# Performance work log

Hardware: AMD Instinct MI355X
Metric: run time of the kernel (lower is better)

The kernel has to match this reference:

```python
import jax
import jax.numpy as jnp
import numpy as np
from jax import lax


def setup_inputs() -> dict:
    key = jax.random.key(0)
    ks = jax.random.split(key, 8)
    B, T, D, H = 65536, 200, 6, 50
    scale1 = 1.0 / np.sqrt(D)
    scale2 = 1.0 / np.sqrt(H)
    return {
        "x0": jax.random.normal(ks[0], (B, T, D), dtype=jnp.float32),
        "t_span": jnp.linspace(0.0, 1.01, 102, dtype=jnp.float32),
        "W1": jax.random.normal(ks[1], (D, H), dtype=jnp.float32) * scale1,
        "b1": jax.random.normal(ks[2], (H,), dtype=jnp.float32) * scale1,
        "W2": jax.random.normal(ks[3], (H, H), dtype=jnp.float32) * scale2,
        "b2": jax.random.normal(ks[4], (H,), dtype=jnp.float32) * scale2,
        "W3": jax.random.normal(ks[5], (H, D), dtype=jnp.float32) * scale2,
        "b3": jax.random.normal(ks[6], (D,), dtype=jnp.float32) * scale2,
    }


def _mlp(y, W1, b1, W2, b2, W3, b3):
    # 3-layer MLP: 6 -> 50 -> 50 -> 6 with ReLU (the ODE dynamics f(t, y))
    h = jax.nn.relu(y @ W1 + b1)
    h = jax.nn.relu(h @ W2 + b2)
    return h @ W3 + b3


def reference(x0, t_span, W1, b1, W2, b2, W3, b3):
    # DimensionalityReduction: AdaptiveAvgPool1d(1) over the time axis == mean over T
    y0 = jnp.mean(x0, axis=1)  # [B, 6]

    def f(y):
        return _mlp(y, W1, b1, W2, b2, W3, b3)

    dts = t_span[1:] - t_span[:-1]  # [101]

    def rk4_step(y, dt):
        k1 = f(y)
        k2 = f(y + 0.5 * dt * k1)
        k3 = f(y + 0.5 * dt * k2)
        k4 = f(y + dt * k3)
        y_next = y + (dt / 6.0) * (k1 + 2.0 * k2 + 2.0 * k3 + k4)
        return y_next, None

    yT, _ = lax.scan(rk4_step, y0, dts)
    return yT  # y[-1], shape [B, 6]
```

## Files before the change

kernel.cpp:

```cpp
#include <hip/hip_runtime.h>
#include <cstdint>


#define D_IN   6
#define H_DIM  50
#define T_LEN  200

typedef const float __attribute__((address_space(4)))* cfp;

__device__ __forceinline__ void mlp_eval(
    cfp W1, cfp b1, cfp W2, cfp b2, cfp W3, cfp b3,
    const float y[D_IN], float k[D_IN])
{
    float h1[H_DIM];
#pragma unroll
    for (int j = 0; j < H_DIM; ++j) h1[j] = b1[j];
#pragma unroll
    for (int i = 0; i < D_IN; ++i) {
        float v = y[i];
#pragma unroll
        for (int j = 0; j < H_DIM; ++j) h1[j] = fmaf(v, W1[i * H_DIM + j], h1[j]);
    }
#pragma unroll
    for (int j = 0; j < H_DIM; ++j) h1[j] = fmaxf(h1[j], 0.0f);

    float h2[H_DIM];
#pragma unroll
    for (int j = 0; j < H_DIM; ++j) h2[j] = b2[j];
#pragma unroll
    for (int i = 0; i < H_DIM; ++i) {
        float v = h1[i];
#pragma unroll
        for (int j = 0; j < H_DIM; ++j) h2[j] = fmaf(v, W2[i * H_DIM + j], h2[j]);
    }

#pragma unroll
    for (int d = 0; d < D_IN; ++d) k[d] = b3[d];
#pragma unroll
    for (int i = 0; i < H_DIM; ++i) {
        float v = fmaxf(h2[i], 0.0f);
#pragma unroll
        for (int d = 0; d < D_IN; ++d) k[d] = fmaf(v, W3[i * D_IN + d], k[d]);
    }
}

extern "C" __global__ __launch_bounds__(256)
void ode_fused(const float* __restrict__ x0, const float* __restrict__ ts_g,
               const float* __restrict__ W1g, const float* __restrict__ b1g,
               const float* __restrict__ W2g, const float* __restrict__ b2g,
               const float* __restrict__ W3g, const float* __restrict__ b3g,
               float* __restrict__ out, int nt)
{
    int b = blockIdx.x * blockDim.x + threadIdx.x;

    cfp W1 = (cfp)(uintptr_t)W1g;
    cfp b1 = (cfp)(uintptr_t)b1g;
    cfp W2 = (cfp)(uintptr_t)W2g;
    cfp b2 = (cfp)(uintptr_t)b2g;
    cfp W3 = (cfp)(uintptr_t)W3g;
    cfp b3 = (cfp)(uintptr_t)b3g;
    cfp ts = (cfp)(uintptr_t)ts_g;

    const float4* xrow = (const float4*)(x0 + (size_t)b * (T_LEN * D_IN));
    float acc[D_IN];
#pragma unroll
    for (int d = 0; d < D_IN; ++d) acc[d] = 0.0f;

#pragma unroll 4
    for (int c = 0; c < (T_LEN * D_IN) / 12; ++c) {
        float4 v0 = xrow[c * 3 + 0];
        float4 v1 = xrow[c * 3 + 1];
        float4 v2 = xrow[c * 3 + 2];
        acc[0] += v0.x + v1.z;
        acc[1] += v0.y + v1.w;
        acc[2] += v0.z + v2.x;
        acc[3] += v0.w + v2.y;
        acc[4] += v1.x + v2.z;
        acc[5] += v1.y + v2.w;
    }

    float y[D_IN];
#pragma unroll
    for (int d = 0; d < D_IN; ++d) y[d] = acc[d] * (1.0f / (float)T_LEN);

#pragma unroll 1
    for (int s = 0; s < nt - 1; ++s) {
        float t0 = ts[s];
        float t1 = ts[s + 1];
        float dt = t1 - t0;

        float acck[D_IN];
        float yt[D_IN];
#pragma unroll
        for (int d = 0; d < D_IN; ++d) { acck[d] = 0.0f; yt[d] = y[d]; }

#pragma unroll 1
        for (int st = 0; st < 4; ++st) {
            float k[D_IN];
            mlp_eval(W1, b1, W2, b2, W3, b3, yt, k);
            float w = (st == 1 || st == 2) ? 2.0f : 1.0f;
            float a = (st == 2) ? 1.0f : 0.5f;
#pragma unroll
            for (int d = 0; d < D_IN; ++d) {
                acck[d] = fmaf(w, k[d], acck[d]);
                yt[d]   = fmaf(a * dt, k[d], y[d]);
            }
        }
#pragma unroll
        for (int d = 0; d < D_IN; ++d) y[d] = fmaf(dt * (1.0f / 6.0f), acck[d], y[d]);
    }

    float* o = out + (size_t)b * D_IN;
#pragma unroll
    for (int d = 0; d < D_IN; ++d) o[d] = y[d];
}

extern "C" void kernel_launch(void* const* d_in, const int* in_sizes, int n_in,
                              void* d_out, int out_size, void* d_ws, size_t ws_size,
                              hipStream_t stream) {
    const float* x0 = (const float*)d_in[0];
    const float* ts = (const float*)d_in[1];
    const float* W1 = (const float*)d_in[2];
    const float* b1 = (const float*)d_in[3];
    const float* W2 = (const float*)d_in[4];
    const float* b2 = (const float*)d_in[5];
    const float* W3 = (const float*)d_in[6];
    const float* b3 = (const float*)d_in[7];
    float* out = (float*)d_out;

    int B  = in_sizes[0] / (T_LEN * D_IN);
    int nt = in_sizes[1];

    dim3 block(256);
    dim3 grid(B / 256);
    hipLaunchKernelGGL(ode_fused, grid, block, 0, stream,
                       x0, ts, W1, b1, W2, b2, W3, b3, out, nt);
}
```

Measured before the change: 4.967 ms.

## Stage padded MLP weights in LDS and spill hidden layer to shared memory

Weights, biases and time points are copied once per block into padded LDS buffers, so the MLP reads weights as broadcast float4 LDS loads instead of scalar constant-memory loads. The first hidden activation is written to a per-thread strided LDS scratch and read back in a partially unrolled loop, which lowers register pressure in the 50x50 layer. The cost is extra LDS traffic per evaluation, about 54KB of LDS per block which limits occupancy, and a __launch_bounds__ hint of one block per CU.

```diff
diff --git a/kernel.cpp b/kernel.cpp
--- a/kernel.cpp
+++ b/kernel.cpp
@@ -3,69 +3,133 @@
 
 
 #define D_IN   6
-#define H_DIM  50
+#define H      50
+#define HP     52
+#define W3P    8
 #define T_LEN  200
-
-typedef const float __attribute__((address_space(4)))* cfp;
+#define NTHR   256
+
+#define OFF_W1 0
+#define OFF_B1 (OFF_W1 + D_IN*HP)
+#define OFF_W2 (OFF_B1 + HP)
+#define OFF_B2 (OFF_W2 + H*HP)
+#define OFF_W3 (OFF_B2 + HP)
+#define OFF_B3 (OFF_W3 + H*W3P)
+#define OFF_TS (OFF_B3 + W3P)
+#define OFF_H1 (OFF_TS + 104)
+#define SMEM_FLOATS (OFF_H1 + H*NTHR)
 
 __device__ __forceinline__ void mlp_eval(
-    cfp W1, cfp b1, cfp W2, cfp b2, cfp W3, cfp b3,
-    const float y[D_IN], float k[D_IN])
+    const float* __restrict__ sm, int tid, const float yt[D_IN], float k[D_IN])
 {
-    float h1[H_DIM];
-#pragma unroll
-    for (int j = 0; j < H_DIM; ++j) h1[j] = b1[j];
-#pragma unroll
-    for (int i = 0; i < D_IN; ++i) {
-        float v = y[i];
-#pragma unroll
-        for (int j = 0; j < H_DIM; ++j) h1[j] = fmaf(v, W1[i * H_DIM + j], h1[j]);
-    }
-#pragma unroll
-    for (int j = 0; j < H_DIM; ++j) h1[j] = fmaxf(h1[j], 0.0f);
-
-    float h2[H_DIM];
-#pragma unroll
-    for (int j = 0; j < H_DIM; ++j) h2[j] = b2[j];
-#pragma unroll
-    for (int i = 0; i < H_DIM; ++i) {
-        float v = h1[i];
-#pragma unroll
-        for (int j = 0; j < H_DIM; ++j) h2[j] = fmaf(v, W2[i * H_DIM + j], h2[j]);
-    }
-
-#pragma unroll
-    for (int d = 0; d < D_IN; ++d) k[d] = b3[d];
-#pragma unroll
-    for (int i = 0; i < H_DIM; ++i) {
+    float h1[HP];
+    {
+        const float4* B1 = (const float4*)(sm + OFF_B1);
+#pragma unroll
+        for (int q = 0; q < HP / 4; ++q) {
+            float4 v = B1[q];
+            h1[4 * q + 0] = v.x; h1[4 * q + 1] = v.y;
+            h1[4 * q + 2] = v.z; h1[4 * q + 3] = v.w;
+        }
+#pragma unroll
+        for (int i = 0; i < D_IN; ++i) {
+            float v = yt[i];
+            const float4* Wr = (const float4*)(sm + OFF_W1 + i * HP);
+#pragma unroll
+            for (int q = 0; q < HP / 4; ++q) {
+                float4 w = Wr[q];
+                h1[4 * q + 0] = fmaf(v, w.x, h1[4 * q + 0]);
+                h1[4 * q + 1] = fmaf(v, w.y, h1[4 * q + 1]);
+                h1[4 * q + 2] = fmaf(v, w.z, h1[4 * q + 2]);
+                h1[4 * q + 3] = fmaf(v, w.w, h1[4 * q + 3]);
+            }
+        }
+    }
+
+    float* e = (float*)(sm + OFF_H1) + tid;
+#pragma unroll
+    for (int j = 0; j < H; ++j) e[j * NTHR] = fmaxf(h1[j], 0.0f);
+
+    float h2[HP];
+    {
+        const float4* B2 = (const float4*)(sm + OFF_B2);
+#pragma unroll
+        for (int q = 0; q < HP / 4; ++q) {
+            float4 v = B2[q];
+            h2[4 * q + 0] = v.x; h2[4 * q + 1] = v.y;
+            h2[4 * q + 2] = v.z; h2[4 * q + 3] = v.w;
+        }
+    }
+#pragma unroll 2
+    for (int i = 0; i < H; ++i) {
+        float v = sm[OFF_H1 + i * NTHR + tid];
+        const float4* Wr = (const float4*)(sm + OFF_W2 + i * HP);
+#pragma unroll
+        for (int q = 0; q < HP / 4; ++q) {
+            float4 w = Wr[q];
+            h2[4 * q + 0] = fmaf(v, w.x, h2[4 * q + 0]);
+            h2[4 * q + 1] = fmaf(v, w.y, h2[4 * q + 1]);
+            h2[4 * q + 2] = fmaf(v, w.z, h2[4 * q + 2]);
+            h2[4 * q + 3] = fmaf(v, w.w, h2[4 * q + 3]);
+        }
+    }
+
+    {
+        const float4* B3 = (const float4*)(sm + OFF_B3);
+        float4 b30 = B3[0], b31 = B3[1];
+        k[0] = b30.x; k[1] = b30.y; k[2] = b30.z;
+        k[3] = b30.w; k[4] = b31.x; k[5] = b31.y;
+    }
+#pragma unroll
+    for (int i = 0; i < H; ++i) {
         float v = fmaxf(h2[i], 0.0f);
-#pragma unroll
-        for (int d = 0; d < D_IN; ++d) k[d] = fmaf(v, W3[i * D_IN + d], k[d]);
+        const float4* Wr = (const float4*)(sm + OFF_W3 + i * W3P);
+        float4 w0 = Wr[0], w1 = Wr[1];
+        k[0] = fmaf(v, w0.x, k[0]);
+        k[1] = fmaf(v, w0.y, k[1]);
+        k[2] = fmaf(v, w0.z, k[2]);
+        k[3] = fmaf(v, w0.w, k[3]);
+        k[4] = fmaf(v, w1.x, k[4]);
+        k[5] = fmaf(v, w1.y, k[5]);
     }
 }
 
-extern "C" __global__ __launch_bounds__(256)
+extern "C" __global__ __launch_bounds__(NTHR, 1)
 void ode_fused(const float* __restrict__ x0, const float* __restrict__ ts_g,
                const float* __restrict__ W1g, const float* __restrict__ b1g,
                const float* __restrict__ W2g, const float* __restrict__ b2g,
                const float* __restrict__ W3g, const float* __restrict__ b3g,
                float* __restrict__ out, int nt)
 {
-    int b = blockIdx.x * blockDim.x + threadIdx.x;
-
-    cfp W1 = (cfp)(uintptr_t)W1g;
-    cfp b1 = (cfp)(uintptr_t)b1g;
-    cfp W2 = (cfp)(uintptr_t)W2g;
-    cfp b2 = (cfp)(uintptr_t)b2g;
-    cfp W3 = (cfp)(uintptr_t)W3g;
-    cfp b3 = (cfp)(uintptr_t)b3g;
-    cfp ts = (cfp)(uintptr_t)ts_g;
+    __shared__ float sm[SMEM_FLOATS];
+    const int tid = threadIdx.x;
+    const int b   = blockIdx.x * NTHR + tid;
+
+    for (int idx = tid; idx < D_IN * HP; idx += NTHR) {
+        int r = idx / HP, c = idx - r * HP;
+        sm[OFF_W1 + idx] = (c < H) ? W1g[r * H + c] : 0.0f;
+    }
+    for (int idx = tid; idx < HP; idx += NTHR)
+        sm[OFF_B1 + idx] = (idx < H) ? b1g[idx] : 0.0f;
+    for (int idx = tid; idx < H * HP; idx += NTHR) {
+        int r = idx / HP, c = idx - r * HP;
+        sm[OFF_W2 + idx] = (c < H) ? W2g[r * H + c] : 0.0f;
+    }
+    for (int idx = tid; idx < HP; idx += NTHR)
+        sm[OFF_B2 + idx] = (idx < H) ? b2g[idx] : 0.0f;
+    for (int idx = tid; idx < H * W3P; idx += NTHR) {
+        int r = idx >> 3, c = idx & 7;
+        sm[OFF_W3 + idx] = (c < D_IN) ? W3g[r * D_IN + c] : 0.0f;
+    }
+    for (int idx = tid; idx < W3P; idx += NTHR)
+        sm[OFF_B3 + idx] = (idx < D_IN) ? b3g[idx] : 0.0f;
+    for (int idx = tid; idx < nt && idx < 104; idx += NTHR)
+        sm[OFF_TS + idx] = ts_g[idx];
 
     const float4* xrow = (const float4*)(x0 + (size_t)b * (T_LEN * D_IN));
     float acc[D_IN];
 #pragma unroll
     for (int d = 0; d < D_IN; ++d) acc[d] = 0.0f;
-
 #pragma unroll 4
     for (int c = 0; c < (T_LEN * D_IN) / 12; ++c) {
         float4 v0 = xrow[c * 3 + 0];
@@ -78,15 +142,16 @@
         acc[4] += v1.x + v2.z;
         acc[5] += v1.y + v2.w;
     }
-
     float y[D_IN];
 #pragma unroll
     for (int d = 0; d < D_IN; ++d) y[d] = acc[d] * (1.0f / (float)T_LEN);
+
+    __syncthreads();
 
 #pragma unroll 1
     for (int s = 0; s < nt - 1; ++s) {
-        float t0 = ts[s];
-        float t1 = ts[s + 1];
+        float t0 = sm[OFF_TS + s];
+        float t1 = sm[OFF_TS + s + 1];
         float dt = t1 - t0;
 
         float acck[D_IN];
@@ -97,7 +162,7 @@
 #pragma unroll 1
         for (int st = 0; st < 4; ++st) {
             float k[D_IN];
-            mlp_eval(W1, b1, W2, b2, W3, b3, yt, k);
+            mlp_eval(sm, tid, yt, k);
             float w = (st == 1 || st == 2) ? 2.0f : 1.0f;
             float a = (st == 2) ? 1.0f : 0.5f;
 #pragma unroll
@@ -131,8 +196,8 @@
     int B  = in_sizes[0] / (T_LEN * D_IN);
     int nt = in_sizes[1];
 
-    dim3 block(256);
-    dim3 grid(B / 256);
+    dim3 block(NTHR);
+    dim3 grid(B / NTHR);
     hipLaunchKernelGGL(ode_fused, grid, block, 0, stream,
                        x0, ts, W1, b1, W2, b2, W3, b3, out, nt);
 }
```

After: 8.404 ms. +69.2%, slower.

## Stage hidden activations in LDS and double-buffer vectorized W2 row-pair loads

Applied to the files above, without the earlier changes.

The MLP evaluation is restructured. Weights are now read as float4 vector loads through plain global pointers instead of scalar constant-address-space loads. The ReLU'd first hidden layer is spilled to a per-thread LDS column so the W2 product can stream two rows at a time through double-buffered register arrays. Launch bounds are raised to allow more registers per thread. The aim is to cut scalar-load instruction overhead and hide weight-load latency. The cost is 50 KB of LDS per block and lower occupancy, and weight loads move from the scalar path to per-lane vector loads.

```diff
diff --git a/kernel.cpp b/kernel.cpp
--- a/kernel.cpp
+++ b/kernel.cpp
@@ -3,69 +3,69 @@
 
 
 #define D_IN   6
-#define H_DIM  50
+#define H      50
 #define T_LEN  200
-
-typedef const float __attribute__((address_space(4)))* cfp;
-
-__device__ __forceinline__ void mlp_eval(
-    cfp W1, cfp b1, cfp W2, cfp b2, cfp W3, cfp b3,
-    const float y[D_IN], float k[D_IN])
+#define NTHR   256
+#define NPAIR  25
+
+__device__ __forceinline__ float f4c(float4 v, int c) {
+    return c == 0 ? v.x : c == 1 ? v.y : c == 2 ? v.z : v.w;
+}
+
+__device__ __forceinline__ void load_pair(float4 (&buf)[NPAIR], const float4* W2f4, int p,
+                                          float& v0, float& v1, const float* echoT)
 {
-    float h1[H_DIM];
-#pragma unroll
-    for (int j = 0; j < H_DIM; ++j) h1[j] = b1[j];
-#pragma unroll
-    for (int i = 0; i < D_IN; ++i) {
-        float v = y[i];
-#pragma unroll
-        for (int j = 0; j < H_DIM; ++j) h1[j] = fmaf(v, W1[i * H_DIM + j], h1[j]);
-    }
-#pragma unroll
-    for (int j = 0; j < H_DIM; ++j) h1[j] = fmaxf(h1[j], 0.0f);
-
-    float h2[H_DIM];
-#pragma unroll
-    for (int j = 0; j < H_DIM; ++j) h2[j] = b2[j];
-#pragma unroll
-    for (int i = 0; i < H_DIM; ++i) {
-        float v = h1[i];
-#pragma unroll
-        for (int j = 0; j < H_DIM; ++j) h2[j] = fmaf(v, W2[i * H_DIM + j], h2[j]);
-    }
-
-#pragma unroll
-    for (int d = 0; d < D_IN; ++d) k[d] = b3[d];
-#pragma unroll
-    for (int i = 0; i < H_DIM; ++i) {
-        float v = fmaxf(h2[i], 0.0f);
-#pragma unroll
-        for (int d = 0; d < D_IN; ++d) k[d] = fmaf(v, W3[i * D_IN + d], k[d]);
-    }
-}
-
-extern "C" __global__ __launch_bounds__(256)
+    const float4* w = W2f4 + p * NPAIR;
+#pragma unroll
+    for (int q = 0; q < NPAIR; ++q) buf[q] = w[q];
+    v0 = echoT[(2 * p) * NTHR];
+    v1 = echoT[(2 * p + 1) * NTHR];
+}
+
+__device__ __forceinline__ void fma_pair(const float4 (&buf)[NPAIR], float v0, float v1,
+                                         float (&h2)[H])
+{
+#pragma unroll
+    for (int q = 0; q < 12; ++q) {
+        h2[4 * q + 0] = fmaf(v0, buf[q].x, h2[4 * q + 0]);
+        h2[4 * q + 1] = fmaf(v0, buf[q].y, h2[4 * q + 1]);
+        h2[4 * q + 2] = fmaf(v0, buf[q].z, h2[4 * q + 2]);
+        h2[4 * q + 3] = fmaf(v0, buf[q].w, h2[4 * q + 3]);
+    }
+    h2[48] = fmaf(v0, buf[12].x, h2[48]);
+    h2[49] = fmaf(v0, buf[12].y, h2[49]);
+    h2[0]  = fmaf(v1, buf[12].z, h2[0]);
+    h2[1]  = fmaf(v1, buf[12].w, h2[1]);
+#pragma unroll
+    for (int q = 13; q < NPAIR; ++q) {
+        int jb = 4 * q - 50;
+        h2[jb + 0] = fmaf(v1, buf[q].x, h2[jb + 0]);
+        h2[jb + 1] = fmaf(v1, buf[q].y, h2[jb + 1]);
+        h2[jb + 2] = fmaf(v1, buf[q].z, h2[jb + 2]);
+        h2[jb + 3] = fmaf(v1, buf[q].w, h2[jb + 3]);
+    }
+}
+
+extern "C" __global__ __launch_bounds__(NTHR, 1)
 void ode_fused(const float* __restrict__ x0, const float* __restrict__ ts_g,
                const float* __restrict__ W1g, const float* __restrict__ b1g,
                const float* __restrict__ W2g, const float* __restrict__ b2g,
                const float* __restrict__ W3g, const float* __restrict__ b3g,
                float* __restrict__ out, int nt)
 {
-    int b = blockIdx.x * blockDim.x + threadIdx.x;
-
-    cfp W1 = (cfp)(uintptr_t)W1g;
-    cfp b1 = (cfp)(uintptr_t)b1g;
-    cfp W2 = (cfp)(uintptr_t)W2g;
-    cfp b2 = (cfp)(uintptr_t)b2g;
-    cfp W3 = (cfp)(uintptr_t)W3g;
-    cfp b3 = (cfp)(uintptr_t)b3g;
-    cfp ts = (cfp)(uintptr_t)ts_g;
+    __shared__ float echo[H * NTHR];
+    const int tid = threadIdx.x;
+    const int b   = blockIdx.x * NTHR + tid;
+    float* echoT  = echo + tid;
+
+    const float4* W1f4 = (const float4*)W1g;
+    const float4* W2f4 = (const float4*)W2g;
+    const float4* W3f4 = (const float4*)W3g;
 
     const float4* xrow = (const float4*)(x0 + (size_t)b * (T_LEN * D_IN));
     float acc[D_IN];
 #pragma unroll
     for (int d = 0; d < D_IN; ++d) acc[d] = 0.0f;
-
 #pragma unroll 4
     for (int c = 0; c < (T_LEN * D_IN) / 12; ++c) {
         float4 v0 = xrow[c * 3 + 0];
@@ -78,15 +78,14 @@
         acc[4] += v1.x + v2.z;
         acc[5] += v1.y + v2.w;
     }
-
     float y[D_IN];
 #pragma unroll
     for (int d = 0; d < D_IN; ++d) y[d] = acc[d] * (1.0f / (float)T_LEN);
 
 #pragma unroll 1
     for (int s = 0; s < nt - 1; ++s) {
-        float t0 = ts[s];
-        float t1 = ts[s + 1];
+        float t0 = ts_g[s];
+        float t1 = ts_g[s + 1];
         float dt = t1 - t0;
 
         float acck[D_IN];
@@ -96,8 +95,98 @@
 
 #pragma unroll 1
         for (int st = 0; st < 4; ++st) {
+            float4 B1[12];
+#pragma unroll
+            for (int q = 0; q < 12; ++q) B1[q] = ((const float4*)b1g)[q];
+            float2 b1t = *(const float2*)(b1g + 48);
+
+            float h1[H];
+#pragma unroll
+            for (int m = 0; m < 75; ++m) {
+                float4 w = W1f4[m];
+#pragma unroll
+                for (int c = 0; c < 4; ++c) {
+                    int e = 4 * m + c;
+                    int i = e / H;
+                    int j = e - H * i;
+                    float bj  = (j < 48) ? f4c(B1[j >> 2], j & 3)
+                                         : (j == 48 ? b1t.x : b1t.y);
+                    float add = (e < H) ? bj : h1[j];
+                    h1[j] = fmaf(yt[i], f4c(w, c), add);
+                }
+            }
+
+#pragma unroll
+            for (int j = 0; j < H; ++j) echoT[j * NTHR] = fmaxf(h1[j], 0.0f);
+
+            float h2[H];
+            {
+                float4 B2[12];
+#pragma unroll
+                for (int q = 0; q < 12; ++q) B2[q] = ((const float4*)b2g)[q];
+                float2 b2t = *(const float2*)(b2g + 48);
+
+                float4 P[NPAIR];
+                float v0, v1;
+                load_pair(P, W2f4, 0, v0, v1, echoT);
+#pragma unroll
+                for (int q = 0; q < 12; ++q) {
+                    h2[4 * q + 0] = fmaf(v0, P[q].x, f4c(B2[q], 0));
+                    h2[4 * q + 1] = fmaf(v0, P[q].y, f4c(B2[q], 1));
+                    h2[4 * q + 2] = fmaf(v0, P[q].z, f4c(B2[q], 2));
+                    h2[4 * q + 3] = fmaf(v0, P[q].w, f4c(B2[q], 3));
+                }
+                h2[48] = fmaf(v0, P[12].x, b2t.x);
+                h2[49] = fmaf(v0, P[12].y, b2t.y);
+                h2[0]  = fmaf(v1, P[12].z, h2[0]);
+                h2[1]  = fmaf(v1, P[12].w, h2[1]);
+#pragma unroll
+                for (int q = 13; q < NPAIR; ++q) {
+                    int jb = 4 * q - 50;
+                    h2[jb + 0] = fmaf(v1, P[q].x, h2[jb + 0]);
+                    h2[jb + 1] = fmaf(v1, P[q].y, h2[jb + 1]);
+                    h2[jb + 2] = fmaf(v1, P[q].z, h2[jb + 2]);
+                    h2[jb + 3] = fmaf(v1, P[q].w, h2[jb + 3]);
+                }
+            }
+            {
+                float4 A[NPAIR], Bb[NPAIR];
+                float v0A, v1A, v0B, v1B;
+                load_pair(A, W2f4, 1, v0A, v1A, echoT);
+#pragma unroll 1
+                for (int it = 0; it < 11; ++it) {
+                    load_pair(Bb, W2f4, 2 * it + 2, v0B, v1B, echoT);
+                    fma_pair(A, v0A, v1A, h2);
+                    load_pair(A, W2f4, 2 * it + 3, v0A, v1A, echoT);
+                    fma_pair(Bb, v0B, v1B, h2);
+                }
+                load_pair(Bb, W2f4, 24, v0B, v1B, echoT);
+                fma_pair(A, v0A, v1A, h2);
+                fma_pair(Bb, v0B, v1B, h2);
+            }
+
+            float h2r[H];
+#pragma unroll
+            for (int j = 0; j < H; ++j) h2r[j] = fmaxf(h2[j], 0.0f);
+
+            float4 b3a = *(const float4*)b3g;
+            float2 b3t = *(const float2*)(b3g + 4);
+
             float k[D_IN];
-            mlp_eval(W1, b1, W2, b2, W3, b3, yt, k);
+#pragma unroll
+            for (int m = 0; m < 75; ++m) {
+                float4 w = W3f4[m];
+#pragma unroll
+                for (int c = 0; c < 4; ++c) {
+                    int e = 4 * m + c;
+                    int i = e / D_IN;
+                    int d = e - D_IN * i;
+                    float bd  = (d < 4) ? f4c(b3a, d) : (d == 4 ? b3t.x : b3t.y);
+                    float add = (e < D_IN) ? bd : k[d];
+                    k[d] = fmaf(h2r[i], f4c(w, c), add);
+                }
+            }
+
             float w = (st == 1 || st == 2) ? 2.0f : 1.0f;
             float a = (st == 2) ? 1.0f : 0.5f;
 #pragma unroll
@@ -131,8 +220,8 @@
     int B  = in_sizes[0] / (T_LEN * D_IN);
     int nt = in_sizes[1];
 
-    dim3 block(256);
-    dim3 grid(B / 256);
+    dim3 block(NTHR);
+    dim3 grid(B / NTHR);
     hipLaunchKernelGGL(ode_fused, grid, block, 0, stream,
                        x0, ts, W1, b1, W2, b2, W3, b3, out, nt);
 }
```

Result: slower. 6.201 ms (+24.8%).
